# Kernel optimization log

Measured on AMD Instinct MI355X. Metric: run time of the kernel, lower is better.

Reference implementation:

```python
import jax, jax.numpy as jnp
import numpy as np

P = 10  # pred_num_conn (capped by max_pred_num_conn), component 0 = background
L = 6   # label_num_conn, component 0 = background
N, H, W = 4, 1024, 1024


def setup_inputs() -> dict:
    key = jax.random.key(0)
    k1, k2, k3 = jax.random.split(key, 3)
    pred = jax.random.uniform(k1, (N, H, W), dtype=jnp.float32)
    pred_conn = jax.random.randint(k2, (N, H, W), 0, P, dtype=jnp.int32)
    label_conn = jax.random.randint(k3, (N, H, W), 0, L, dtype=jnp.int32)
    return {"pred": pred, "pred_conn": pred_conn, "label_conn": label_conn}


def _image_sc_loss(pred_i, pconn, lconn):
    # pred_i: [H,W] float, pconn/lconn: [H,W] int component ids
    ph = jax.nn.one_hot(pconn, P, dtype=pred_i.dtype)   # [H,W,P]
    lh = jax.nn.one_hot(lconn, L, dtype=pred_i.dtype)   # [H,W,L]
    pm = ph * pred_i[..., None]                          # pred_j = mask_j * pred
    inter = jnp.einsum('hwl,hwp->lp', lh, pm)            # [L,P] intersection areas
    pred_area = jnp.sum(pm, axis=(0, 1))                 # [P]
    label_area = jnp.sum(lh, axis=(0, 1))                # [L]
    union = label_area[:, None] + pred_area[None, :] - inter
    safe_union = jnp.where(union == 0, 1.0, union)
    # compute_iou: 0 if intersect==0, 1 if union==0, else inter/union
    iou = jnp.where(inter == 0, 0.0,
                    jnp.where(union == 0, 1.0, inter / safe_union))
    ious = iou[1:, 1:]                                   # drop background comps -> [L-1, P-1]
    pair_conn = jnp.sum(ious, axis=1)                    # sum of nonzero ious per label comp
    pair_num = jnp.sum(ious != 0, axis=1).astype(pred_i.dtype)
    contrib = jnp.where(pair_num > 0,
                        pair_conn / jnp.where(pair_num > 0, pair_num, 1.0), 0.0)
    pair_conn_sum = jnp.sum(contrib)
    pred_col_sum = jnp.sum(ious, axis=0)                 # [P-1]
    lone_pred_num = jnp.sum(pred_col_sum == 0).astype(pred_i.dtype)
    real_label_num = jnp.asarray(L - 1, pred_i.dtype)
    img_connectivity = pair_conn_sum / (real_label_num + lone_pred_num)
    return 1.0 - img_connectivity                        # sc_loss for one class (class_num=1)


def reference(pred, pred_conn, label_conn):
    sc = jax.vmap(_image_sc_loss)(pred, pred_conn, label_conn)  # [N]
    return jnp.mean(sc)
```

## Files before the change

### kernel.cpp

```cpp
#include <hip/hip_runtime.h>

#define PP 10
#define LL 6
#define NIMG 4
#define HW (1024*1024)
#define BINS 66
#define BX 128
#define TPB 256
#define ITERS (HW / 4 / (BX * TPB))


__global__ __launch_bounds__(TPB) void accum_kernel(
    const float* __restrict__ pred,
    const int*   __restrict__ pconn,
    const int*   __restrict__ lconn,
    float*       __restrict__ ws)
{
    __shared__ float sb[BINS * TPB];

    const int tid = threadIdx.x;
    const int img = blockIdx.y;
    const size_t base = (size_t)img * HW;

    {
        float4* sb4 = (float4*)sb;
        const int n4 = BINS * TPB / 4;
        for (int i = tid; i < n4; i += TPB) sb4[i] = make_float4(0.f, 0.f, 0.f, 0.f);
    }
    __syncthreads();

    const float4* __restrict__ p4  = (const float4*)(pred  + base);
    const int4*   __restrict__ pc4 = (const int4*)(pconn + base);
    const int4*   __restrict__ lc4 = (const int4*)(lconn + base);

    const int v0 = blockIdx.x * TPB + tid;
    const int stride = BX * TPB;

    float4 p[ITERS]; int4 pc[ITERS], lc[ITERS];
#pragma unroll
    for (int i = 0; i < ITERS; ++i) {
        const int v = v0 + i * stride;
        p[i]  = p4[v];
        pc[i] = pc4[v];
        lc[i] = lc4[v];
    }

#pragma unroll
    for (int i = 0; i < ITERS; ++i) {
        atomicAdd(&sb[(lc[i].x * PP + pc[i].x) * TPB + tid], p[i].x);
        atomicAdd(&sb[(60 + lc[i].x) * TPB + tid], 1.0f);
        atomicAdd(&sb[(lc[i].y * PP + pc[i].y) * TPB + tid], p[i].y);
        atomicAdd(&sb[(60 + lc[i].y) * TPB + tid], 1.0f);
        atomicAdd(&sb[(lc[i].z * PP + pc[i].z) * TPB + tid], p[i].z);
        atomicAdd(&sb[(60 + lc[i].z) * TPB + tid], 1.0f);
        atomicAdd(&sb[(lc[i].w * PP + pc[i].w) * TPB + tid], p[i].w);
        atomicAdd(&sb[(60 + lc[i].w) * TPB + tid], 1.0f);
    }
    __syncthreads();

    float* wout = ws + ((size_t)img * BX + blockIdx.x) * BINS;

    {
        const int b = tid >> 2, q = tid & 3;
        const float* col = sb + b * TPB + 64 * q;
        float s = 0.0f;
#pragma unroll
        for (int i = 0; i < 16; ++i) {
            const int ii = ((i + tid) & 15) * 4;
            const float4 t4 = *(const float4*)(col + ii);
            s += t4.x + t4.y + t4.z + t4.w;
        }
        s += __shfl_down(s, 1, 64);
        s += __shfl_down(s, 2, 64);
        if (q == 0) wout[b] = s;
    }
    if (tid < 8) {
        const int b = 64 + (tid >> 2), q = tid & 3;
        const float* col = sb + b * TPB + 64 * q;
        float s = 0.0f;
#pragma unroll
        for (int i = 0; i < 16; ++i) {
            const float4 t4 = *(const float4*)(col + i * 4);
            s += t4.x + t4.y + t4.z + t4.w;
        }
        s += __shfl_down(s, 1, 64);
        s += __shfl_down(s, 2, 64);
        if (q == 0) wout[b] = s;
    }
}

__global__ __launch_bounds__(320) void finalize_kernel(
    const float* __restrict__ ws, float* __restrict__ out)
{
    __shared__ float red[NIMG * BINS];
    __shared__ float contrib[NIMG];
    const int t = threadIdx.x;

    if (t < NIMG * BINS) {
        const int img = t / BINS, b = t % BINS;
        const float* base = ws + (size_t)img * BX * BINS + b;
        float s = 0.0f;
#pragma unroll 8
        for (int bx = 0; bx < BX; ++bx) s += base[bx * BINS];
        red[t] = s;
    }
    __syncthreads();

    if (t < NIMG) {
        const float* b = red + t * BINS;
        float inter[LL][PP];
        float pred_area[PP];
        float label_area[LL];
        for (int p = 0; p < PP; ++p) pred_area[p] = 0.0f;
        for (int l = 0; l < LL; ++l) {
            label_area[l] = b[60 + l];
            for (int p = 0; p < PP; ++p) {
                inter[l][p] = b[l * PP + p];
                pred_area[p] += inter[l][p];
            }
        }
        float ious[LL][PP];
        for (int l = 1; l < LL; ++l) {
            for (int p = 1; p < PP; ++p) {
                float in = inter[l][p];
                float un = label_area[l] + pred_area[p] - in;
                float iou;
                if (in == 0.0f)      iou = 0.0f;
                else if (un == 0.0f) iou = 1.0f;
                else                 iou = in / un;
                ious[l][p] = iou;
            }
        }
        float pair_conn_sum = 0.0f;
        for (int l = 1; l < LL; ++l) {
            float pc = 0.0f; int pn = 0;
            for (int p = 1; p < PP; ++p) {
                pc += ious[l][p];
                pn += (ious[l][p] != 0.0f) ? 1 : 0;
            }
            if (pn > 0) pair_conn_sum += pc / (float)pn;
        }
        int lone = 0;
        for (int p = 1; p < PP; ++p) {
            float cs = 0.0f;
            for (int l = 1; l < LL; ++l) cs += ious[l][p];
            lone += (cs == 0.0f) ? 1 : 0;
        }
        contrib[t] = 1.0f - pair_conn_sum / (5.0f + (float)lone);
    }
    __syncthreads();

    if (t == 0)
        out[0] = (contrib[0] + contrib[1] + contrib[2] + contrib[3]) * 0.25f;
}

extern "C" void kernel_launch(void* const* d_in, const int* in_sizes, int n_in,
                              void* d_out, int out_size, void* d_ws, size_t ws_size,
                              hipStream_t stream) {
    const float* pred  = (const float*)d_in[0];
    const int*   pconn = (const int*)d_in[1];
    const int*   lconn = (const int*)d_in[2];
    float* out = (float*)d_out;
    float* ws  = (float*)d_ws;

    dim3 grid(BX, NIMG);
    accum_kernel<<<grid, TPB, 0, stream>>>(pred, pconn, lconn, ws);

    finalize_kernel<<<1, 320, 0, stream>>>(ws, out);
}
```

Baseline: 129.4 us.

## Use more smaller blocks, register label counts, plain LDS adds, split finalize reduction

```diff
diff --git a/kernel.cpp b/kernel.cpp
--- a/kernel.cpp
+++ b/kernel.cpp
@@ -5,18 +5,20 @@
 #define NIMG 4
 #define HW (1024*1024)
 #define BINS 66
-#define BX 128
-#define TPB 256
-#define ITERS (HW / 4 / (BX * TPB))
+#define NB 60
+#define BX 512
+#define TPB 128
+#define ITERS 4
 
 
-__global__ __launch_bounds__(TPB) void accum_kernel(
+__global__ __launch_bounds__(TPB, 2) void accum_kernel(
     const float* __restrict__ pred,
     const int*   __restrict__ pconn,
     const int*   __restrict__ lconn,
     float*       __restrict__ ws)
 {
-    __shared__ float sb[BINS * TPB];
+    __shared__ float sb[NB * TPB];
+    __shared__ float scnt[2][8];
 
     const int tid = threadIdx.x;
     const int img = blockIdx.y;
@@ -24,8 +26,8 @@
 
     {
         float4* sb4 = (float4*)sb;
-        const int n4 = BINS * TPB / 4;
-        for (int i = tid; i < n4; i += TPB) sb4[i] = make_float4(0.f, 0.f, 0.f, 0.f);
+        for (int i = tid; i < NB * TPB / 4; i += TPB)
+            sb4[i] = make_float4(0.f, 0.f, 0.f, 0.f);
     }
     __syncthreads();
 
@@ -45,75 +47,82 @@
         lc[i] = lc4[v];
     }
 
+    float cnt[LL];
+#pragma unroll
+    for (int l = 0; l < LL; ++l) cnt[l] = 0.0f;
+
 #pragma unroll
     for (int i = 0; i < ITERS; ++i) {
-        atomicAdd(&sb[(lc[i].x * PP + pc[i].x) * TPB + tid], p[i].x);
-        atomicAdd(&sb[(60 + lc[i].x) * TPB + tid], 1.0f);
-        atomicAdd(&sb[(lc[i].y * PP + pc[i].y) * TPB + tid], p[i].y);
-        atomicAdd(&sb[(60 + lc[i].y) * TPB + tid], 1.0f);
-        atomicAdd(&sb[(lc[i].z * PP + pc[i].z) * TPB + tid], p[i].z);
-        atomicAdd(&sb[(60 + lc[i].z) * TPB + tid], 1.0f);
-        atomicAdd(&sb[(lc[i].w * PP + pc[i].w) * TPB + tid], p[i].w);
-        atomicAdd(&sb[(60 + lc[i].w) * TPB + tid], 1.0f);
+#pragma unroll
+        for (int l = 0; l < LL; ++l)
+            cnt[l] += (float)((lc[i].x == l) + (lc[i].y == l)
+                            + (lc[i].z == l) + (lc[i].w == l));
+        sb[(lc[i].x * PP + pc[i].x) * TPB + tid] += p[i].x;
+        sb[(lc[i].y * PP + pc[i].y) * TPB + tid] += p[i].y;
+        sb[(lc[i].z * PP + pc[i].z) * TPB + tid] += p[i].z;
+        sb[(lc[i].w * PP + pc[i].w) * TPB + tid] += p[i].w;
     }
     __syncthreads();
 
     float* wout = ws + ((size_t)img * BX + blockIdx.x) * BINS;
 
+#pragma unroll
+    for (int l = 0; l < LL; ++l) {
+        float s = cnt[l];
+        s += __shfl_down(s, 32, 64); s += __shfl_down(s, 16, 64);
+        s += __shfl_down(s,  8, 64); s += __shfl_down(s,  4, 64);
+        s += __shfl_down(s,  2, 64); s += __shfl_down(s,  1, 64);
+        if ((tid & 63) == 0) scnt[tid >> 6][l] = s;
+    }
+
     {
-        const int b = tid >> 2, q = tid & 3;
-        const float* col = sb + b * TPB + 64 * q;
-        float s = 0.0f;
+        const int b = tid >> 1, h = tid & 1;
+        if (b < NB) {
+            const float* col = sb + b * TPB + 64 * h;
+            float s = 0.0f;
 #pragma unroll
-        for (int i = 0; i < 16; ++i) {
-            const int ii = ((i + tid) & 15) * 4;
-            const float4 t4 = *(const float4*)(col + ii);
-            s += t4.x + t4.y + t4.z + t4.w;
+            for (int i = 0; i < 16; ++i) {
+                const int ii = ((i + tid) & 15) * 4;
+                const float4 t4 = *(const float4*)(col + ii);
+                s += t4.x + t4.y + t4.z + t4.w;
+            }
+            s += __shfl_down(s, 1, 64);
+            if (h == 0) wout[b] = s;
         }
-        s += __shfl_down(s, 1, 64);
-        s += __shfl_down(s, 2, 64);
-        if (q == 0) wout[b] = s;
     }
-    if (tid < 8) {
-        const int b = 64 + (tid >> 2), q = tid & 3;
-        const float* col = sb + b * TPB + 64 * q;
-        float s = 0.0f;
-#pragma unroll
-        for (int i = 0; i < 16; ++i) {
-            const float4 t4 = *(const float4*)(col + i * 4);
-            s += t4.x + t4.y + t4.z + t4.w;
-        }
-        s += __shfl_down(s, 1, 64);
-        s += __shfl_down(s, 2, 64);
-        if (q == 0) wout[b] = s;
-    }
+    __syncthreads();
+    if (tid < LL) wout[NB + tid] = scnt[0][tid] + scnt[1][tid];
 }
 
-__global__ __launch_bounds__(320) void finalize_kernel(
+__global__ __launch_bounds__(1024) void finalize_kernel(
     const float* __restrict__ ws, float* __restrict__ out)
 {
+    __shared__ float part[4][NIMG * BINS];
     __shared__ float red[NIMG * BINS];
     __shared__ float contrib[NIMG];
     const int t = threadIdx.x;
 
-    if (t < NIMG * BINS) {
-        const int img = t / BINS, b = t % BINS;
-        const float* base = ws + (size_t)img * BX * BINS + b;
+    for (int T = t; T < 4 * NIMG * BINS; T += 1024) {
+        const int ib = T >> 2, sub = T & 3;
+        const int img = ib / BINS, b = ib % BINS;
+        const float* basep = ws + ((size_t)img * BX + sub) * BINS + b;
         float s = 0.0f;
 #pragma unroll 8
-        for (int bx = 0; bx < BX; ++bx) s += base[bx * BINS];
-        red[t] = s;
+        for (int j = 0; j < BX / 4; ++j) s += basep[(size_t)j * 4 * BINS];
+        part[sub][ib] = s;
     }
+    __syncthreads();
+
+    if (t < NIMG * BINS)
+        red[t] = part[0][t] + part[1][t] + part[2][t] + part[3][t];
     __syncthreads();
 
     if (t < NIMG) {
         const float* b = red + t * BINS;
-        float inter[LL][PP];
-        float pred_area[PP];
-        float label_area[LL];
+        float inter[LL][PP], pred_area[PP], label_area[LL];
         for (int p = 0; p < PP; ++p) pred_area[p] = 0.0f;
         for (int l = 0; l < LL; ++l) {
-            label_area[l] = b[60 + l];
+            label_area[l] = b[NB + l];
             for (int p = 0; p < PP; ++p) {
                 inter[l][p] = b[l * PP + p];
                 pred_area[p] += inter[l][p];
@@ -149,7 +158,6 @@
         contrib[t] = 1.0f - pair_conn_sum / (5.0f + (float)lone);
     }
     __syncthreads();
-
     if (t == 0)
         out[0] = (contrib[0] + contrib[1] + contrib[2] + contrib[3]) * 0.25f;
 }
@@ -166,5 +174,5 @@
     dim3 grid(BX, NIMG);
     accum_kernel<<<grid, TPB, 0, stream>>>(pred, pconn, lconn, ws);
 
-    finalize_kernel<<<1, 320, 0, stream>>>(ws, out);
+    finalize_kernel<<<1, 1024, 0, stream>>>(ws, out);
 }
```

Result: faster. 109.6 us (-15.3%).
